# Kernel optimization log

Measured on AMD Instinct MI355X. Metric: run time of the kernel, lower is better.

Reference implementation:

```python
import jax, jax.numpy as jnp
import numpy as np

N = 100000
E = 1600000
IN_CH, H1, H2 = 128, 128, 64


def gcn_conv(x, edge_index, W, b):
    """PyG GCNConv: add self-loops, symmetric normalization, linear + scatter-add."""
    n = x.shape[0]
    row, col = edge_index[0], edge_index[1]
    loop = jnp.arange(n, dtype=edge_index.dtype)
    row = jnp.concatenate([row, loop])  # sources (incl. self loops)
    col = jnp.concatenate([col, loop])  # targets
    h = x @ W                           # [n, out]
    deg = jax.ops.segment_sum(jnp.ones(row.shape[0], dtype=x.dtype), col, num_segments=n)
    dinv = jnp.where(deg > 0, jax.lax.rsqrt(deg), jnp.zeros((), dtype=x.dtype))
    norm = dinv[row] * dinv[col]        # [E+n]
    out = jax.ops.segment_sum(norm[:, None] * h[row], col, num_segments=n)
    return out + b


def setup_inputs() -> dict:
    key = jax.random.key(0)
    ks = jax.random.split(key, 8)
    x = jax.random.normal(ks[0], (N, IN_CH), dtype=jnp.float32)
    edge_index = jax.random.randint(ks[1], (2, E), 0, N, dtype=jnp.int32)
    batch = jnp.zeros((N,), dtype=jnp.int32)
    W1 = jax.random.normal(ks[2], (IN_CH, H1), dtype=jnp.float32) * 0.05
    b1 = jnp.zeros((H1,), dtype=jnp.float32)
    Wmu = jax.random.normal(ks[3], (H1, H2), dtype=jnp.float32) * 0.05
    bmu = jnp.zeros((H2,), dtype=jnp.float32)
    Wls = jax.random.normal(ks[4], (H1, H2), dtype=jnp.float32) * 0.05
    bls = jnp.zeros((H2,), dtype=jnp.float32)
    return {"x": x, "edge_index": edge_index, "batch": batch,
            "W1": W1, "b1": b1, "Wmu": Wmu, "bmu": bmu, "Wls": Wls, "bls": bls}


def reference(x, edge_index, batch, W1, b1, Wmu, bmu, Wls, bls):
    # classifier is None (use_classify=False), dropout=0 -> pure GCN path
    h = jax.nn.relu(gcn_conv(x, edge_index, W1, b1))
    mu = gcn_conv(h, edge_index, Wmu, bmu)
    logstd = gcn_conv(h, edge_index, Wls, bls)
    return (mu, logstd)
```

## Files before the change

### kernel.cpp

```cpp
#include <hip/hip_runtime.h>
#include <hip/hip_bf16.h>


#define BW_SH   8
#define BW      (1 << BW_SH)
#define NBUCK_MAX 512
#define EPB     6144
#define CAP     5120
#define GPAD    16

typedef __attribute__((ext_vector_type(8))) short bf16x8;
typedef __attribute__((ext_vector_type(4))) float f32x4;

__device__ __forceinline__ unsigned bf16rne(float f) {
    unsigned u = __float_as_uint(f);
    return (u + 0x7fffu + ((u >> 16) & 1u)) >> 16;
}
__device__ __forceinline__ float bflo(unsigned u) { return __uint_as_float(u << 16); }
__device__ __forceinline__ float bfhi(unsigned u) { return __uint_as_float(u & 0xffff0000u); }

__global__ void k_wprep(const float* __restrict__ W1,
                        const float* __restrict__ Wmu, const float* __restrict__ Wls,
                        const float* __restrict__ bmu, const float* __restrict__ bls,
                        unsigned short* __restrict__ W1t,
                        unsigned short* __restrict__ Wct,
                        float* __restrict__ bcat,
                        int* __restrict__ gcur, int nbuck) {
    int b = blockIdx.x, t = threadIdx.x;
    if (b < 128) {
        W1t[b * 128 + t] = (unsigned short)bf16rne(W1[t * 128 + b]);
        if (b == 0) bcat[t] = (t < 64) ? bmu[t] : bls[t - 64];
    } else if (b < 256) {
        int c = b - 128;
        float w = (c < 64) ? Wmu[t * 64 + c] : Wls[t * 64 + (c - 64)];
        Wct[c * 128 + t] = (unsigned short)bf16rne(w);
    } else {
        int idx = (b - 256) * 128 + t;
        if (idx < nbuck) gcur[idx * GPAD] = idx * CAP;
    }
}

__global__ __launch_bounds__(256) void k_bg1(
    const int* __restrict__ row, const int* __restrict__ col, int e,
    int* __restrict__ gcur, int* __restrict__ pairs,
    const float* __restrict__ X, const unsigned short* __restrict__ W1t,
    unsigned* __restrict__ Hbf, int n, int nbb)
{
    extern __shared__ char dsm[];
    int tid = threadIdx.x;
    if (blockIdx.x < nbb) {
        int* items = (int*)dsm;
        unsigned short* bkt = (unsigned short*)(dsm + 24576);
        int* hcnt  = (int*)(dsm + 24576 + 12288);
        int* lbase = hcnt + NBUCK_MAX;
        int e0 = blockIdx.x * EPB;
        int e1 = min(e, e0 + EPB);
        int m = e1 - e0;
        for (int b = tid; b < NBUCK_MAX; b += 256) hcnt[b] = 0;
        __syncthreads();
        for (int i = tid; i < m; i += 256) {
            int s = row[e0 + i];
            int d = col[e0 + i];
            items[i] = (s << BW_SH) | (d & (BW - 1));
            int b = d >> BW_SH;
            bkt[i] = (unsigned short)b;
            atomicAdd(&hcnt[b], 1);
        }
        __syncthreads();
        for (int b = tid; b < NBUCK_MAX; b += 256)
            lbase[b] = hcnt[b] ? atomicAdd(&gcur[b * GPAD], hcnt[b]) : 0;
        __syncthreads();
        for (int i = tid; i < m; i += 256) {
            int pos = atomicAdd(&lbase[bkt[i]], 1);
            pairs[pos] = items[i];
        }
    } else {
        unsigned short* ot = (unsigned short*)dsm;
        int w = tid >> 6, L = tid & 63;
        int q = L >> 4, ml = L & 15;
        int nb0 = (blockIdx.x - nbb) * 64 + w * 16;
        int node = nb0 + ml;
        bool valid = node < n;
        const bf16x8* Bp = (const bf16x8*)W1t;
        f32x4 acc[8];
        #pragma unroll
        for (int cb = 0; cb < 8; ++cb) { acc[cb][0]=0.f; acc[cb][1]=0.f; acc[cb][2]=0.f; acc[cb][3]=0.f; }
        #pragma unroll
        for (int kc = 0; kc < 4; ++kc) {
            bf16x8 af = {0,0,0,0,0,0,0,0};
            if (valid) {
                const float4* xp = (const float4*)&X[(size_t)node * 128 + kc * 32 + q * 8];
                float4 xa = xp[0], xb = xp[1];
                af[0] = (short)bf16rne(xa.x); af[1] = (short)bf16rne(xa.y);
                af[2] = (short)bf16rne(xa.z); af[3] = (short)bf16rne(xa.w);
                af[4] = (short)bf16rne(xb.x); af[5] = (short)bf16rne(xb.y);
                af[6] = (short)bf16rne(xb.z); af[7] = (short)bf16rne(xb.w);
            }
            #pragma unroll
            for (int cb = 0; cb < 8; ++cb) {
                bf16x8 bfr = Bp[(cb * 16 + ml) * 16 + kc * 4 + q];
                acc[cb] = __builtin_amdgcn_mfma_f32_16x16x32_bf16(af, bfr, acc[cb], 0, 0, 0);
            }
        }
        #pragma unroll
        for (int cb = 0; cb < 8; ++cb)
            #pragma unroll
            for (int r = 0; r < 4; ++r)
                ot[(w * 16 + q * 4 + r) * 136 + cb * 16 + ml] =
                    (unsigned short)bf16rne(acc[cb][r]);
        __syncthreads();
        #pragma unroll
        for (int it = 0; it < 4; ++it) {
            int flat = it * 64 + L;
            int rw = flat >> 4, cg = flat & 15;
            int nd = nb0 + rw;
            if (nd < n) {
                uint4 v = *(const uint4*)&ot[(w * 16 + rw) * 136 + cg * 8];
                *(uint4*)&Hbf[(size_t)nd * 64 + cg * 4] = v;
            }
        }
    }
}

__global__ __launch_bounds__(256) void k_fill5(
    const int* __restrict__ gcur, const int* __restrict__ pairs,
    int* __restrict__ offs, int* __restrict__ cnt, float* __restrict__ dinv,
    int* __restrict__ esrc, int n)
{
    __shared__ int lcnt[BW];
    __shared__ int lcur[BW];
    __shared__ int wsum[4];
    __shared__ int lesrc[CAP];
    int b = blockIdx.x, tid = threadIdx.x;
    int t0 = b << BW_SH;
    int nt = min(n - t0, BW);
    int base = b * CAP;
    int m = min(gcur[b * GPAD] - base, CAP);
    lcnt[tid] = 0;
    __syncthreads();
    for (int i = tid; i < m; i += 256)
        atomicAdd(&lcnt[pairs[base + i] & (BW - 1)], 1);
    __syncthreads();
    int s = lcnt[tid];
    int x = s;
    #pragma unroll
    for (int d = 1; d < 64; d <<= 1) {
        int t = __shfl_up(x, d);
        if ((tid & 63) >= d) x += t;
    }
    if ((tid & 63) == 63) wsum[tid >> 6] = x;
    __syncthreads();
    int pre = 0;
    #pragma unroll
    for (int i = 0; i < 4; ++i)
        if (i < (tid >> 6)) pre += wsum[i];
    int ex = pre + x - s;
    lcur[tid] = ex;
    __syncthreads();
    if (tid < nt) {
        offs[t0 + tid] = base + ex;
        cnt[t0 + tid]  = s;
        dinv[t0 + tid] = 1.0f / sqrtf((float)(s + 1));
    }
    for (int i = tid; i < m; i += 256) {
        int it = pairs[base + i];
        int pos = atomicAdd(&lcur[it & (BW - 1)], 1);
        lesrc[pos] = it >> BW_SH;
    }
    __syncthreads();
    for (int i = tid; i < m; i += 256)
        esrc[base + i] = lesrc[i];
}

__global__ __launch_bounds__(256) void k_prop_bf2(
    const unsigned* __restrict__ hbf, const float* __restrict__ dinv,
    const int* __restrict__ offs, const int* __restrict__ cnt,
    const int* __restrict__ esrc,
    unsigned* __restrict__ out_bf,
    const float* __restrict__ bias, int do_relu, int n)
{
    int wid = (blockIdx.x * blockDim.x + threadIdx.x) >> 6;
    int v0  = wid * 2;
    if (v0 >= n) return;
    int v1  = v0 + 1;
    bool hasB = v1 < n;
    int lane = threadIdx.x & 63;
    int half = lane >> 5;
    int fl   = lane & 31;
    const uint2* rows = (const uint2*)hbf;

    float dvA = dinv[v0];
    int   stA = offs[v0], dgA = cnt[v0];
    float dvB = hasB ? dinv[v1] : 0.f;
    int   stB = hasB ? offs[v1] : 0;
    int   dgB = hasB ? cnt[v1]  : 0;

    float aA0=0.f,aA1=0.f,aA2=0.f,aA3=0.f;
    float aB0=0.f,aB1=0.f,aB2=0.f,aB3=0.f;
    if (half == 0) {
        uint2 r = rows[(size_t)v0 * 32 + fl];
        aA0 = dvA * bflo(r.x); aA1 = dvA * bfhi(r.x);
        aA2 = dvA * bflo(r.y); aA3 = dvA * bfhi(r.y);
    } else if (hasB) {
        uint2 r = rows[(size_t)v1 * 32 + fl];
        aB0 = dvB * bflo(r.x); aB1 = dvB * bfhi(r.x);
        aB2 = dvB * bflo(r.y); aB3 = dvB * bfhi(r.y);
    }

    int dmax = max(dgA, dgB);
    for (int base = 0; base < dmax; base += 64) {
        int mA = dgA - base;
        int mB = dgB - base;
        int sA = 0, sB = 0; float wA = 0.f, wB = 0.f;
        if (lane < mA) { sA = esrc[stA + base + lane]; wA = dinv[sA]; }
        if (lane < mB) { sB = esrc[stB + base + lane]; wB = dinv[sB]; }
        int mm = min(max(mA, mB), 64);
        for (int j = 0; j < mm; j += 8) {
            int siA[4], siB[4]; float wiA[4], wiB[4]; uint2 rA[4], rB[4];
            #pragma unroll
            for (int u = 0; u < 4; ++u) {
                siA[u] = __shfl(sA, j + 2 * u + half);
                wiA[u] = __shfl(wA, j + 2 * u + half);
                siB[u] = __shfl(sB, j + 2 * u + half);
                wiB[u] = __shfl(wB, j + 2 * u + half);
            }
            #pragma unroll
            for (int u = 0; u < 4; ++u) {
                rA[u] = rows[(size_t)siA[u] * 32 + fl];
                rB[u] = rows[(size_t)siB[u] * 32 + fl];
            }
            #pragma unroll
            for (int u = 0; u < 4; ++u) {
                aA0 = fmaf(wiA[u], bflo(rA[u].x), aA0);
                aA1 = fmaf(wiA[u], bfhi(rA[u].x), aA1);
                aA2 = fmaf(wiA[u], bflo(rA[u].y), aA2);
                aA3 = fmaf(wiA[u], bfhi(rA[u].y), aA3);
                aB0 = fmaf(wiB[u], bflo(rB[u].x), aB0);
                aB1 = fmaf(wiB[u], bfhi(rB[u].x), aB1);
                aB2 = fmaf(wiB[u], bflo(rB[u].y), aB2);
                aB3 = fmaf(wiB[u], bfhi(rB[u].y), aB3);
            }
        }
    }
    aA0 += __shfl_xor(aA0, 32); aA1 += __shfl_xor(aA1, 32);
    aA2 += __shfl_xor(aA2, 32); aA3 += __shfl_xor(aA3, 32);
    aB0 += __shfl_xor(aB0, 32); aB1 += __shfl_xor(aB1, 32);
    aB2 += __shfl_xor(aB2, 32); aB3 += __shfl_xor(aB3, 32);

    float c0, c1, c2, c3, dv; int vout;
    if (half == 0) { c0=aA0; c1=aA1; c2=aA2; c3=aA3; dv=dvA; vout=v0; }
    else           { c0=aB0; c1=aB1; c2=aB2; c3=aB3; dv=dvB; vout=v1; }
    if (half == 0 || hasB) {
        c0 *= dv; c1 *= dv; c2 *= dv; c3 *= dv;
        if (bias) {
            c0 += bias[fl * 4 + 0]; c1 += bias[fl * 4 + 1];
            c2 += bias[fl * 4 + 2]; c3 += bias[fl * 4 + 3];
        }
        if (do_relu) {
            c0 = fmaxf(c0, 0.f); c1 = fmaxf(c1, 0.f);
            c2 = fmaxf(c2, 0.f); c3 = fmaxf(c3, 0.f);
        }
        uint2 pk;
        pk.x = (bf16rne(c1) << 16) | bf16rne(c0);
        pk.y = (bf16rne(c3) << 16) | bf16rne(c2);
        ((uint2*)out_bf)[(size_t)vout * 32 + fl] = pk;
    }
}

__global__ __launch_bounds__(256) void k_gemm2(
    const unsigned* __restrict__ Gbf, const unsigned short* __restrict__ Wct,
    const float* __restrict__ bcat, float* __restrict__ out, int n)
{
    __shared__ float ot[4][16][132];
    int tid = threadIdx.x;
    int w = tid >> 6, L = tid & 63;
    int q = L >> 4, ml = L & 15;
    int nb0 = blockIdx.x * 64 + w * 16;
    int node = nb0 + ml;
    bool valid = node < n;
    const bf16x8* Ap = (const bf16x8*)Gbf;
    const bf16x8* Bp = (const bf16x8*)Wct;
    f32x4 acc[8];
    #pragma unroll
    for (int cb = 0; cb < 8; ++cb) { acc[cb][0]=0.f; acc[cb][1]=0.f; acc[cb][2]=0.f; acc[cb][3]=0.f; }
    #pragma unroll
    for (int kc = 0; kc < 4; ++kc) {
        bf16x8 af = {0,0,0,0,0,0,0,0};
        if (valid) af = Ap[(size_t)node * 16 + kc * 4 + q];
        #pragma unroll
        for (int cb = 0; cb < 8; ++cb) {
            bf16x8 bfr = Bp[(cb * 16 + ml) * 16 + kc * 4 + q];
            acc[cb] = __builtin_amdgcn_mfma_f32_16x16x32_bf16(af, bfr, acc[cb], 0, 0, 0);
        }
    }
    #pragma unroll
    for (int cb = 0; cb < 8; ++cb)
        #pragma unroll
        for (int r = 0; r < 4; ++r)
            ot[w][q * 4 + r][cb * 16 + ml] = acc[cb][r];
    __syncthreads();
    #pragma unroll
    for (int it = 0; it < 8; ++it) {
        int flat = it * 64 + L;
        int row = flat >> 5, c4 = flat & 31;
        int col = c4 * 4;
        int nd = nb0 + row;
        if (nd < n) {
            float4 v = *(const float4*)&ot[w][row][col];
            float4 bb = *(const float4*)&bcat[col];
            f32x4 vv;
            vv[0] = v.x + bb.x; vv[1] = v.y + bb.y;
            vv[2] = v.z + bb.z; vv[3] = v.w + bb.w;
            size_t off = (col < 64)
                ? ((size_t)nd * 64 + col)
                : ((size_t)n * 64 + (size_t)nd * 64 + (col - 64));
            __builtin_nontemporal_store(vv, (f32x4*)&out[off]);
        }
    }
}

extern "C" void kernel_launch(void* const* d_in, const int* in_sizes, int n_in,
                              void* d_out, int out_size, void* d_ws, size_t ws_size,
                              hipStream_t stream) {
    const float* x   = (const float*)d_in[0];
    const int*   ei  = (const int*)d_in[1];
    const float* W1  = (const float*)d_in[3];
    const float* b1  = (const float*)d_in[4];
    const float* Wmu = (const float*)d_in[5];
    const float* bmu = (const float*)d_in[6];
    const float* Wls = (const float*)d_in[7];
    const float* bls = (const float*)d_in[8];
    float* out = (float*)d_out;

    int n = in_sizes[0] / 128;
    int e = in_sizes[1] / 2;
    const int* erow = ei;
    const int* ecol = ei + e;
    int nbuck = (n + BW - 1) >> BW_SH;
    int nbb   = (e + EPB - 1) / EPB;

    char* p = (char*)d_ws;
    auto alloc = [&](size_t bytes) -> char* {
        char* q = p; p += (bytes + 255) & ~(size_t)255; return q;
    };
    int*            gcur  = (int*)           alloc((size_t)NBUCK_MAX * GPAD * 4);
    int*            cnt   = (int*)           alloc((size_t)n * 4);
    int*            offs  = (int*)           alloc((size_t)n * 4);
    float*          dinv  = (float*)         alloc((size_t)n * 4);
    int*            esrc  = (int*)           alloc((size_t)nbuck * CAP * 4);
    unsigned short* W1t   = (unsigned short*)alloc(128 * 128 * 2);
    unsigned short* Wct   = (unsigned short*)alloc(128 * 128 * 2);
    float*          bcat  = (float*)         alloc(128 * 4);
    unsigned*       hbf   = (unsigned*)      alloc((size_t)n * 64 * 4);
    unsigned*       h1bf  = (unsigned*)      alloc((size_t)n * 64 * 4);
    unsigned*       gbf   = (unsigned*)      alloc((size_t)n * 64 * 4);
    int*            pairs = (int*)gbf;

    k_wprep<<<260, 128, 0, stream>>>(W1, Wmu, Wls, bmu, bls, W1t, Wct, bcat,
                                     gcur, nbuck);
    k_bg1<<<nbb + (n + 63) / 64, 256, 40960, stream>>>(
        erow, ecol, e, gcur, pairs, x, W1t, hbf, n, nbb);
    k_fill5<<<nbuck, 256, 0, stream>>>(gcur, pairs, offs, cnt, dinv, esrc, n);

    int nwaves = (n + 1) / 2;
    int pblocks = (nwaves + 3) / 4;
    k_prop_bf2<<<pblocks, 256, 0, stream>>>(hbf, dinv, offs, cnt, esrc,
                                            h1bf, b1, 1, n);
    k_prop_bf2<<<pblocks, 256, 0, stream>>>(h1bf, dinv, offs, cnt, esrc,
                                            gbf, nullptr, 0, n);
    k_gemm2<<<(n + 63) / 64, 256, 0, stream>>>(gbf, Wct, bcat, out, n);
}
```

Before: 319.5 us.

## Restructure preprocessing: merge weight prep into bucketing, fuse fill with layer-1 GEMM

Replaces the three-kernel preprocessing chain (weight prep, bucket+GEMM, fill) with two kernels. Edge bucketing now recomputes from vectorized int4 row/col loads instead of staging items in LDS, and absorbs the weight transposes. The per-bucket CSR fill is fused with the X·W1 GEMM, so the GEMM overlaps the fill instead of the bucketing pass. A memset replaces the gcur initialization, edges per block are doubled, and the aim is fewer launches and better overlap at the cost of re-reading col and row.

```diff
diff --git a/kernel.cpp b/kernel.cpp
--- a/kernel.cpp
+++ b/kernel.cpp
@@ -5,7 +5,7 @@
 #define BW_SH   8
 #define BW      (1 << BW_SH)
 #define NBUCK_MAX 512
-#define EPB     6144
+#define EPB     12288
 #define CAP     5120
 #define GPAD    16
 
@@ -19,66 +19,151 @@
 __device__ __forceinline__ float bflo(unsigned u) { return __uint_as_float(u << 16); }
 __device__ __forceinline__ float bfhi(unsigned u) { return __uint_as_float(u & 0xffff0000u); }
 
-__global__ void k_wprep(const float* __restrict__ W1,
-                        const float* __restrict__ Wmu, const float* __restrict__ Wls,
-                        const float* __restrict__ bmu, const float* __restrict__ bls,
-                        unsigned short* __restrict__ W1t,
-                        unsigned short* __restrict__ Wct,
-                        float* __restrict__ bcat,
-                        int* __restrict__ gcur, int nbuck) {
-    int b = blockIdx.x, t = threadIdx.x;
-    if (b < 128) {
-        W1t[b * 128 + t] = (unsigned short)bf16rne(W1[t * 128 + b]);
-        if (b == 0) bcat[t] = (t < 64) ? bmu[t] : bls[t - 64];
-    } else if (b < 256) {
-        int c = b - 128;
-        float w = (c < 64) ? Wmu[t * 64 + c] : Wls[t * 64 + (c - 64)];
-        Wct[c * 128 + t] = (unsigned short)bf16rne(w);
-    } else {
-        int idx = (b - 256) * 128 + t;
-        if (idx < nbuck) gcur[idx * GPAD] = idx * CAP;
-    }
-}
-
-__global__ __launch_bounds__(256) void k_bg1(
+__global__ __launch_bounds__(256) void k_pre(
     const int* __restrict__ row, const int* __restrict__ col, int e,
     int* __restrict__ gcur, int* __restrict__ pairs,
+    const float* __restrict__ W1,
+    const float* __restrict__ Wmu, const float* __restrict__ Wls,
+    const float* __restrict__ bmu, const float* __restrict__ bls,
+    unsigned short* __restrict__ W1t, unsigned short* __restrict__ Wct,
+    float* __restrict__ bcat, int nbb)
+{
+    int tid = threadIdx.x;
+    if (blockIdx.x < nbb) {
+        __shared__ int hcnt[NBUCK_MAX];
+        __shared__ int lbase[NBUCK_MAX];
+        int e0 = blockIdx.x * EPB;
+        int m  = min(e - e0, EPB);
+        for (int b = tid; b < NBUCK_MAX; b += 256) hcnt[b] = 0;
+        __syncthreads();
+        int m4 = m >> 2;
+        const int4* c4p = (const int4*)(col + e0);
+        for (int i = tid; i < m4; i += 256) {
+            int4 c4 = c4p[i];
+            atomicAdd(&hcnt[c4.x >> BW_SH], 1);
+            atomicAdd(&hcnt[c4.y >> BW_SH], 1);
+            atomicAdd(&hcnt[c4.z >> BW_SH], 1);
+            atomicAdd(&hcnt[c4.w >> BW_SH], 1);
+        }
+        for (int i = (m4 << 2) + tid; i < m; i += 256)
+            atomicAdd(&hcnt[col[e0 + i] >> BW_SH], 1);
+        __syncthreads();
+        for (int b = tid; b < NBUCK_MAX; b += 256) {
+            int c = hcnt[b];
+            lbase[b] = c ? (b * CAP + atomicAdd(&gcur[b * GPAD], c)) : 0;
+        }
+        __syncthreads();
+        const int4* r4p = (const int4*)(row + e0);
+        for (int i = tid; i < m4; i += 256) {
+            int4 c4 = c4p[i];
+            int4 r4 = r4p[i];
+            int pos;
+            pos = atomicAdd(&lbase[c4.x >> BW_SH], 1);
+            pairs[pos] = (r4.x << BW_SH) | (c4.x & (BW - 1));
+            pos = atomicAdd(&lbase[c4.y >> BW_SH], 1);
+            pairs[pos] = (r4.y << BW_SH) | (c4.y & (BW - 1));
+            pos = atomicAdd(&lbase[c4.z >> BW_SH], 1);
+            pairs[pos] = (r4.z << BW_SH) | (c4.z & (BW - 1));
+            pos = atomicAdd(&lbase[c4.w >> BW_SH], 1);
+            pairs[pos] = (r4.w << BW_SH) | (c4.w & (BW - 1));
+        }
+        for (int i = (m4 << 2) + tid; i < m; i += 256) {
+            int c = col[e0 + i], r = row[e0 + i];
+            int pos = atomicAdd(&lbase[c >> BW_SH], 1);
+            pairs[pos] = (r << BW_SH) | (c & (BW - 1));
+        }
+    } else {
+        int w   = blockIdx.x - nbb;
+        int sub = w * 2 + (tid >> 7);
+        int t   = tid & 127;
+        if (sub < 128) {
+            W1t[sub * 128 + t] = (unsigned short)bf16rne(W1[t * 128 + sub]);
+            if (sub == 0) bcat[t] = (t < 64) ? bmu[t] : bls[t - 64];
+        } else {
+            int c = sub - 128;
+            float wv = (c < 64) ? Wmu[t * 64 + c] : Wls[t * 64 + (c - 64)];
+            Wct[c * 128 + t] = (unsigned short)bf16rne(wv);
+        }
+    }
+}
+
+__global__ __launch_bounds__(256) void k_gf(
+    const int* __restrict__ gcur, const int* __restrict__ pairs,
+    int* __restrict__ offs, int* __restrict__ cnt, float* __restrict__ dinv,
+    int* __restrict__ esrc,
     const float* __restrict__ X, const unsigned short* __restrict__ W1t,
-    unsigned* __restrict__ Hbf, int n, int nbb)
+    unsigned* __restrict__ Hbf, int n, int nfb)
 {
     extern __shared__ char dsm[];
     int tid = threadIdx.x;
-    if (blockIdx.x < nbb) {
-        int* items = (int*)dsm;
-        unsigned short* bkt = (unsigned short*)(dsm + 24576);
-        int* hcnt  = (int*)(dsm + 24576 + 12288);
-        int* lbase = hcnt + NBUCK_MAX;
-        int e0 = blockIdx.x * EPB;
-        int e1 = min(e, e0 + EPB);
-        int m = e1 - e0;
-        for (int b = tid; b < NBUCK_MAX; b += 256) hcnt[b] = 0;
-        __syncthreads();
-        for (int i = tid; i < m; i += 256) {
-            int s = row[e0 + i];
-            int d = col[e0 + i];
-            items[i] = (s << BW_SH) | (d & (BW - 1));
-            int b = d >> BW_SH;
-            bkt[i] = (unsigned short)b;
-            atomicAdd(&hcnt[b], 1);
-        }
-        __syncthreads();
-        for (int b = tid; b < NBUCK_MAX; b += 256)
-            lbase[b] = hcnt[b] ? atomicAdd(&gcur[b * GPAD], hcnt[b]) : 0;
-        __syncthreads();
-        for (int i = tid; i < m; i += 256) {
-            int pos = atomicAdd(&lbase[bkt[i]], 1);
-            pairs[pos] = items[i];
-        }
+    if (blockIdx.x < nfb) {
+        int* lcnt  = (int*)dsm;
+        int* lcur  = (int*)(dsm + 1024);
+        int* wsum  = (int*)(dsm + 2048);
+        int* lesrc = (int*)(dsm + 2064);
+        int b = blockIdx.x;
+        int t0 = b << BW_SH;
+        int nt = min(n - t0, BW);
+        int base = b * CAP;
+        int m = min(gcur[b * GPAD], CAP);
+        lcnt[tid] = 0;
+        __syncthreads();
+        int m4 = m >> 2;
+        const int4* p4 = (const int4*)(pairs + base);
+        for (int i = tid; i < m4; i += 256) {
+            int4 v = p4[i];
+            atomicAdd(&lcnt[v.x & (BW - 1)], 1);
+            atomicAdd(&lcnt[v.y & (BW - 1)], 1);
+            atomicAdd(&lcnt[v.z & (BW - 1)], 1);
+            atomicAdd(&lcnt[v.w & (BW - 1)], 1);
+        }
+        for (int i = (m4 << 2) + tid; i < m; i += 256)
+            atomicAdd(&lcnt[pairs[base + i] & (BW - 1)], 1);
+        __syncthreads();
+        int s = lcnt[tid];
+        int x = s;
+        #pragma unroll
+        for (int d = 1; d < 64; d <<= 1) {
+            int t = __shfl_up(x, d);
+            if ((tid & 63) >= d) x += t;
+        }
+        if ((tid & 63) == 63) wsum[tid >> 6] = x;
+        __syncthreads();
+        int pre = 0;
+        #pragma unroll
+        for (int i = 0; i < 4; ++i)
+            if (i < (tid >> 6)) pre += wsum[i];
+        int ex = pre + x - s;
+        lcur[tid] = ex;
+        __syncthreads();
+        if (tid < nt) {
+            offs[t0 + tid] = base + ex;
+            cnt[t0 + tid]  = s;
+            dinv[t0 + tid] = 1.0f / sqrtf((float)(s + 1));
+        }
+        for (int i = tid; i < m4; i += 256) {
+            int4 v = p4[i];
+            int pos;
+            pos = atomicAdd(&lcur[v.x & (BW - 1)], 1); lesrc[pos] = v.x >> BW_SH;
+            pos = atomicAdd(&lcur[v.y & (BW - 1)], 1); lesrc[pos] = v.y >> BW_SH;
+            pos = atomicAdd(&lcur[v.z & (BW - 1)], 1); lesrc[pos] = v.z >> BW_SH;
+            pos = atomicAdd(&lcur[v.w & (BW - 1)], 1); lesrc[pos] = v.w >> BW_SH;
+        }
+        for (int i = (m4 << 2) + tid; i < m; i += 256) {
+            int it = pairs[base + i];
+            int pos = atomicAdd(&lcur[it & (BW - 1)], 1);
+            lesrc[pos] = it >> BW_SH;
+        }
+        __syncthreads();
+        int mc = (m + 3) >> 2;
+        int4* e4 = (int4*)(esrc + base);
+        const int4* l4 = (const int4*)lesrc;
+        for (int i = tid; i < mc; i += 256) e4[i] = l4[i];
     } else {
         unsigned short* ot = (unsigned short*)dsm;
         int w = tid >> 6, L = tid & 63;
         int q = L >> 4, ml = L & 15;
-        int nb0 = (blockIdx.x - nbb) * 64 + w * 16;
+        int nb0 = (blockIdx.x - nfb) * 64 + w * 16;
         int node = nb0 + ml;
         bool valid = node < n;
         const bf16x8* Bp = (const bf16x8*)W1t;
@@ -120,56 +205,6 @@
             }
         }
     }
-}
-
-__global__ __launch_bounds__(256) void k_fill5(
-    const int* __restrict__ gcur, const int* __restrict__ pairs,
-    int* __restrict__ offs, int* __restrict__ cnt, float* __restrict__ dinv,
-    int* __restrict__ esrc, int n)
-{
-    __shared__ int lcnt[BW];
-    __shared__ int lcur[BW];
-    __shared__ int wsum[4];
-    __shared__ int lesrc[CAP];
-    int b = blockIdx.x, tid = threadIdx.x;
-    int t0 = b << BW_SH;
-    int nt = min(n - t0, BW);
-    int base = b * CAP;
-    int m = min(gcur[b * GPAD] - base, CAP);
-    lcnt[tid] = 0;
-    __syncthreads();
-    for (int i = tid; i < m; i += 256)
-        atomicAdd(&lcnt[pairs[base + i] & (BW - 1)], 1);
-    __syncthreads();
-    int s = lcnt[tid];
-    int x = s;
-    #pragma unroll
-    for (int d = 1; d < 64; d <<= 1) {
-        int t = __shfl_up(x, d);
-        if ((tid & 63) >= d) x += t;
-    }
-    if ((tid & 63) == 63) wsum[tid >> 6] = x;
-    __syncthreads();
-    int pre = 0;
-    #pragma unroll
-    for (int i = 0; i < 4; ++i)
-        if (i < (tid >> 6)) pre += wsum[i];
-    int ex = pre + x - s;
-    lcur[tid] = ex;
-    __syncthreads();
-    if (tid < nt) {
-        offs[t0 + tid] = base + ex;
-        cnt[t0 + tid]  = s;
-        dinv[t0 + tid] = 1.0f / sqrtf((float)(s + 1));
-    }
-    for (int i = tid; i < m; i += 256) {
-        int it = pairs[base + i];
-        int pos = atomicAdd(&lcur[it & (BW - 1)], 1);
-        lesrc[pos] = it >> BW_SH;
-    }
-    __syncthreads();
-    for (int i = tid; i < m; i += 256)
-        esrc[base + i] = lesrc[i];
 }
 
 __global__ __launch_bounds__(256) void k_prop_bf2(
@@ -356,11 +391,15 @@
     unsigned*       gbf   = (unsigned*)      alloc((size_t)n * 64 * 4);
     int*            pairs = (int*)gbf;
 
-    k_wprep<<<260, 128, 0, stream>>>(W1, Wmu, Wls, bmu, bls, W1t, Wct, bcat,
-                                     gcur, nbuck);
-    k_bg1<<<nbb + (n + 63) / 64, 256, 40960, stream>>>(
-        erow, ecol, e, gcur, pairs, x, W1t, hbf, n, nbb);
-    k_fill5<<<nbuck, 256, 0, stream>>>(gcur, pairs, offs, cnt, dinv, esrc, n);
+    hipMemsetAsync(gcur, 0, (size_t)NBUCK_MAX * GPAD * 4, stream);
+
+    k_pre<<<nbb + 128, 256, 0, stream>>>(erow, ecol, e, gcur, pairs,
+                                         W1, Wmu, Wls, bmu, bls,
+                                         W1t, Wct, bcat, nbb);
+
+    int ngb = (n + 63) / 64;
+    k_gf<<<nbuck + ngb, 256, 22656, stream>>>(gcur, pairs, offs, cnt, dinv,
+                                              esrc, x, W1t, hbf, n, nbuck);
 
     int nwaves = (n + 1) / 2;
     int pblocks = (nwaves + 3) / 4;
```

Result: slower. 334.1 us (+4.6%).

## Split feature matrix into two column slabs and propagate each slab separately

Applied to the files above, without the earlier changes.

Stores the bf16 hidden feature matrices as two slabs of 64 columns, each contiguous over nodes, in place of one interleaved 128-column row. The propagation kernel now launches twice as many blocks, and each block handles one slab, so every gathered row is 128 bytes instead of 256. The aim is a smaller per-slab working set that fits better in cache during the random neighbor gathers. The cost is that edge indices and dinv are read twice, and the GEMM kernels' addressing changes to match. Edge-index loads also become nontemporal.

```diff
diff --git a/kernel.cpp b/kernel.cpp
--- a/kernel.cpp
+++ b/kernel.cpp
@@ -116,7 +116,7 @@
             int nd = nb0 + rw;
             if (nd < n) {
                 uint4 v = *(const uint4*)&ot[(w * 16 + rw) * 136 + cg * 8];
-                *(uint4*)&Hbf[(size_t)nd * 64 + cg * 4] = v;
+                *(uint4*)&Hbf[((size_t)(cg >> 3) * n + nd) * 32 + (cg & 7) * 4] = v;
             }
         }
     }
@@ -172,14 +172,15 @@
         esrc[base + i] = lesrc[i];
 }
 
-__global__ __launch_bounds__(256) void k_prop_bf2(
+__global__ __launch_bounds__(256) void k_prop_sl(
     const unsigned* __restrict__ hbf, const float* __restrict__ dinv,
     const int* __restrict__ offs, const int* __restrict__ cnt,
     const int* __restrict__ esrc,
     unsigned* __restrict__ out_bf,
     const float* __restrict__ bias, int do_relu, int n)
 {
-    int wid = (blockIdx.x * blockDim.x + threadIdx.x) >> 6;
+    int sl  = blockIdx.x & 1;
+    int wid = (blockIdx.x >> 1) * 4 + (threadIdx.x >> 6);
     int v0  = wid * 2;
     if (v0 >= n) return;
     int v1  = v0 + 1;
@@ -187,7 +188,7 @@
     int lane = threadIdx.x & 63;
     int half = lane >> 5;
     int fl   = lane & 31;
-    const uint2* rows = (const uint2*)hbf;
+    const unsigned* rows = hbf + (size_t)sl * n * 32;
 
     float dvA = dinv[v0];
     int   stA = offs[v0], dgA = cnt[v0];
@@ -195,16 +196,13 @@
     int   stB = hasB ? offs[v1] : 0;
     int   dgB = hasB ? cnt[v1]  : 0;
 
-    float aA0=0.f,aA1=0.f,aA2=0.f,aA3=0.f;
-    float aB0=0.f,aB1=0.f,aB2=0.f,aB3=0.f;
+    float aA0 = 0.f, aA1 = 0.f, aB0 = 0.f, aB1 = 0.f;
     if (half == 0) {
-        uint2 r = rows[(size_t)v0 * 32 + fl];
-        aA0 = dvA * bflo(r.x); aA1 = dvA * bfhi(r.x);
-        aA2 = dvA * bflo(r.y); aA3 = dvA * bfhi(r.y);
+        unsigned r = rows[(unsigned)(v0 * 32 + fl)];
+        aA0 = dvA * bflo(r); aA1 = dvA * bfhi(r);
     } else if (hasB) {
-        uint2 r = rows[(size_t)v1 * 32 + fl];
-        aB0 = dvB * bflo(r.x); aB1 = dvB * bfhi(r.x);
-        aB2 = dvB * bflo(r.y); aB3 = dvB * bfhi(r.y);
+        unsigned r = rows[(unsigned)(v1 * 32 + fl)];
+        aB0 = dvB * bflo(r); aB1 = dvB * bfhi(r);
     }
 
     int dmax = max(dgA, dgB);
@@ -212,11 +210,17 @@
         int mA = dgA - base;
         int mB = dgB - base;
         int sA = 0, sB = 0; float wA = 0.f, wB = 0.f;
-        if (lane < mA) { sA = esrc[stA + base + lane]; wA = dinv[sA]; }
-        if (lane < mB) { sB = esrc[stB + base + lane]; wB = dinv[sB]; }
+        if (lane < mA) {
+            sA = __builtin_nontemporal_load(&esrc[stA + base + lane]);
+            wA = dinv[sA];
+        }
+        if (lane < mB) {
+            sB = __builtin_nontemporal_load(&esrc[stB + base + lane]);
+            wB = dinv[sB];
+        }
         int mm = min(max(mA, mB), 64);
         for (int j = 0; j < mm; j += 8) {
-            int siA[4], siB[4]; float wiA[4], wiB[4]; uint2 rA[4], rB[4];
+            int siA[4], siB[4]; float wiA[4], wiB[4]; unsigned rA[4], rB[4];
             #pragma unroll
             for (int u = 0; u < 4; ++u) {
                 siA[u] = __shfl(sA, j + 2 * u + half);
@@ -226,44 +230,33 @@
             }
             #pragma unroll
             for (int u = 0; u < 4; ++u) {
-                rA[u] = rows[(size_t)siA[u] * 32 + fl];
-                rB[u] = rows[(size_t)siB[u] * 32 + fl];
+                rA[u] = rows[(unsigned)(siA[u] * 32 + fl)];
+                rB[u] = rows[(unsigned)(siB[u] * 32 + fl)];
             }
             #pragma unroll
             for (int u = 0; u < 4; ++u) {
-                aA0 = fmaf(wiA[u], bflo(rA[u].x), aA0);
-                aA1 = fmaf(wiA[u], bfhi(rA[u].x), aA1);
-                aA2 = fmaf(wiA[u], bflo(rA[u].y), aA2);
-                aA3 = fmaf(wiA[u], bfhi(rA[u].y), aA3);
-                aB0 = fmaf(wiB[u], bflo(rB[u].x), aB0);
-                aB1 = fmaf(wiB[u], bfhi(rB[u].x), aB1);
-                aB2 = fmaf(wiB[u], bflo(rB[u].y), aB2);
-                aB3 = fmaf(wiB[u], bfhi(rB[u].y), aB3);
+                aA0 = fmaf(wiA[u], bflo(rA[u]), aA0);
+                aA1 = fmaf(wiA[u], bfhi(rA[u]), aA1);
+                aB0 = fmaf(wiB[u], bflo(rB[u]), aB0);
+                aB1 = fmaf(wiB[u], bfhi(rB[u]), aB1);
             }
         }
     }
     aA0 += __shfl_xor(aA0, 32); aA1 += __shfl_xor(aA1, 32);
-    aA2 += __shfl_xor(aA2, 32); aA3 += __shfl_xor(aA3, 32);
     aB0 += __shfl_xor(aB0, 32); aB1 += __shfl_xor(aB1, 32);
-    aB2 += __shfl_xor(aB2, 32); aB3 += __shfl_xor(aB3, 32);
-
-    float c0, c1, c2, c3, dv; int vout;
-    if (half == 0) { c0=aA0; c1=aA1; c2=aA2; c3=aA3; dv=dvA; vout=v0; }
-    else           { c0=aB0; c1=aB1; c2=aB2; c3=aB3; dv=dvB; vout=v1; }
+
+    float c0, c1, dv; int vout;
+    if (half == 0) { c0 = aA0; c1 = aA1; dv = dvA; vout = v0; }
+    else           { c0 = aB0; c1 = aB1; dv = dvB; vout = v1; }
     if (half == 0 || hasB) {
-        c0 *= dv; c1 *= dv; c2 *= dv; c3 *= dv;
+        c0 *= dv; c1 *= dv;
         if (bias) {
-            c0 += bias[fl * 4 + 0]; c1 += bias[fl * 4 + 1];
-            c2 += bias[fl * 4 + 2]; c3 += bias[fl * 4 + 3];
-        }
-        if (do_relu) {
-            c0 = fmaxf(c0, 0.f); c1 = fmaxf(c1, 0.f);
-            c2 = fmaxf(c2, 0.f); c3 = fmaxf(c3, 0.f);
-        }
-        uint2 pk;
-        pk.x = (bf16rne(c1) << 16) | bf16rne(c0);
-        pk.y = (bf16rne(c3) << 16) | bf16rne(c2);
-        ((uint2*)out_bf)[(size_t)vout * 32 + fl] = pk;
+            c0 += bias[sl * 64 + fl * 2 + 0];
+            c1 += bias[sl * 64 + fl * 2 + 1];
+        }
+        if (do_relu) { c0 = fmaxf(c0, 0.f); c1 = fmaxf(c1, 0.f); }
+        unsigned pk = (bf16rne(c1) << 16) | bf16rne(c0);
+        (out_bf + (size_t)sl * n * 32)[(unsigned)(vout * 32 + fl)] = pk;
     }
 }
 
@@ -286,7 +279,10 @@
     #pragma unroll
     for (int kc = 0; kc < 4; ++kc) {
         bf16x8 af = {0,0,0,0,0,0,0,0};
-        if (valid) af = Ap[(size_t)node * 16 + kc * 4 + q];
+        if (valid) {
+            int cc = kc * 4 + q;
+            af = Ap[((size_t)(cc >> 3) * n + node) * 8 + (cc & 7)];
+        }
         #pragma unroll
         for (int cb = 0; cb < 8; ++cb) {
             bf16x8 bfr = Bp[(cb * 16 + ml) * 16 + kc * 4 + q];
@@ -364,9 +360,9 @@
 
     int nwaves = (n + 1) / 2;
     int pblocks = (nwaves + 3) / 4;
-    k_prop_bf2<<<pblocks, 256, 0, stream>>>(hbf, dinv, offs, cnt, esrc,
-                                            h1bf, b1, 1, n);
-    k_prop_bf2<<<pblocks, 256, 0, stream>>>(h1bf, dinv, offs, cnt, esrc,
-                                            gbf, nullptr, 0, n);
+    k_prop_sl<<<pblocks * 2, 256, 0, stream>>>(hbf, dinv, offs, cnt, esrc,
+                                               h1bf, b1, 1, n);
+    k_prop_sl<<<pblocks * 2, 256, 0, stream>>>(h1bf, dinv, offs, cnt, esrc,
+                                               gbf, nullptr, 0, n);
     k_gemm2<<<(n + 63) / 64, 256, 0, stream>>>(gbf, Wct, bcat, out, n);
 }
```

Measured after the change: 339.3 us. 6.2% more time.
